# Kernel tuning notes

Hardware: AMD Instinct MI355X
Metric: run time of the kernel (lower is better)

## Reference

```python
import jax, jax.numpy as jnp
import numpy as np

D_MODEL = 1024
N_HEADS = 16
HEAD_DIM = D_MODEL // N_HEADS  # 64
WINDOW = 15
NUM_RANDOM = 2
B, L = 2, 2048


def setup_inputs() -> dict:
    key = jax.random.key(0)
    ks = jax.random.split(key, 5)
    x = jax.random.normal(ks[0], (B, L, D_MODEL), dtype=jnp.float32)
    # rotary angles: theta[t, j] = t / 10000^(2j/head_dim), shape [1, L, head_dim//2]
    inv_freq = 1.0 / (10000.0 ** (jnp.arange(0, HEAD_DIM, 2, dtype=jnp.float32) / HEAD_DIM))
    t = jnp.arange(L, dtype=jnp.float32)
    freqs = (t[:, None] * inv_freq[None, :])[None].astype(jnp.float32)  # [1,L,32]
    scale = 0.02
    wq = jax.random.normal(ks[1], (D_MODEL, D_MODEL), dtype=jnp.float32) * scale
    wk = jax.random.normal(ks[2], (D_MODEL, D_MODEL), dtype=jnp.float32) * scale
    wv = jax.random.normal(ks[3], (D_MODEL, D_MODEL), dtype=jnp.float32) * scale
    wo = jax.random.normal(ks[4], (D_MODEL, D_MODEL), dtype=jnp.float32) * scale
    return {"x": x, "freqs": freqs, "wq": wq, "wk": wk, "wv": wv, "wo": wo}


def _rope(t, cos, sin):
    # t: [B,H,L,hd]; interpret last dim as (hd/2, 2) complex pairs and rotate.
    tr = t.reshape(*t.shape[:-1], -1, 2)
    re, im = tr[..., 0], tr[..., 1]
    out_re = re * cos - im * sin
    out_im = re * sin + im * cos
    return jnp.stack([out_re, out_im], axis=-1).reshape(t.shape)


def _bigbird_mask(Lq):
    ii = jnp.arange(Lq)[:, None]
    jj = jnp.arange(Lq)[None, :]
    causal = jj <= ii
    window = jnp.abs(ii - jj) <= (WINDOW // 2)
    glob = (ii == 0) | (jj == 0)
    # random mask: per row i, NUM_RANDOM indices uniform in [0, i]
    rkey = jax.random.key(42)
    u = jax.random.uniform(rkey, (Lq, NUM_RANDOM))
    ridx = jnp.floor(u * (jnp.arange(Lq, dtype=jnp.float32)[:, None] + 1.0)).astype(jnp.int32)
    rmask = jnp.zeros((Lq, Lq), dtype=bool).at[jnp.arange(Lq)[:, None], ridx].set(True)
    # rows with <= NUM_RANDOM causal options attend to all of them
    rmask = rmask | (causal & (ii < NUM_RANDOM))
    return (causal & (window | rmask)) | glob  # [L,L]


def reference(x, freqs, wq, wk, wv, wo):
    b, l, _ = x.shape
    q = (x @ wq.T).reshape(b, l, N_HEADS, HEAD_DIM).transpose(0, 2, 1, 3)  # [B,H,L,hd]
    k = (x @ wk.T).reshape(b, l, N_HEADS, HEAD_DIM).transpose(0, 2, 1, 3)
    v = (x @ wv.T).reshape(b, l, N_HEADS, HEAD_DIM).transpose(0, 2, 1, 3)
    cos = jnp.cos(freqs[:, :l])[:, None]  # [1,1,L,hd/2]
    sin = jnp.sin(freqs[:, :l])[:, None]
    q = _rope(q, cos, sin)
    k = _rope(k, cos, sin)
    attn_mask = _bigbird_mask(l)  # [L,L], broadcast over B,H
    scale = 1.0 / jnp.sqrt(jnp.float32(HEAD_DIM))
    scores = jnp.einsum("bhqd,bhkd->bhqk", q, k) * scale
    scores = jnp.where(attn_mask[None, None], scores, jnp.finfo(scores.dtype).min)
    p = jax.nn.softmax(scores, axis=-1)
    out = jnp.einsum("bhqk,bhkd->bhqd", p, v)
    out = out.transpose(0, 2, 1, 3).reshape(b, l, D_MODEL)
    return out @ wo.T
```

## Files before the change

kernel.cpp:

```cpp
#include <hip/hip_runtime.h>
#include <math.h>

#define SEQ_L 2048
#define DM 1024
#define NH 16
#define HD 64
#define NB 2
#define KD 1024
#define ND 1024

typedef __bf16 bf16;
typedef __bf16 bf16x8 __attribute__((ext_vector_type(8)));
typedef __bf16 bf16x4 __attribute__((ext_vector_type(4)));
typedef __bf16 bf16x2 __attribute__((ext_vector_type(2)));
typedef float f32x4 __attribute__((ext_vector_type(4)));

__device__ inline uint32_t rotl32(uint32_t v, int n) { return (v << n) | (v >> (32 - n)); }

__device__ inline void threefry(uint32_t x0, uint32_t x1, uint32_t* o0, uint32_t* o1) {
  const uint32_t ks0 = 0u, ks1 = 42u, ks2 = 0u ^ 42u ^ 0x1BD11BDAu;
  x0 += ks0; x1 += ks1;
#define TF_R(rr) { x0 += x1; x1 = rotl32(x1, rr); x1 ^= x0; }
  TF_R(13) TF_R(15) TF_R(26) TF_R(6)
  x0 += ks1; x1 += ks2 + 1u;
  TF_R(17) TF_R(29) TF_R(16) TF_R(24)
  x0 += ks2; x1 += ks0 + 2u;
  TF_R(13) TF_R(15) TF_R(26) TF_R(6)
  x0 += ks0; x1 += ks1 + 3u;
  TF_R(17) TF_R(29) TF_R(16) TF_R(24)
  x0 += ks1; x1 += ks2 + 4u;
  TF_R(13) TF_R(15) TF_R(26) TF_R(6)
  x0 += ks2; x1 += ks0 + 5u;
#undef TF_R
  *o0 = x0; *o1 = x1;
}

__device__ inline int rand_col(int i, int s) {
  uint32_t o0, o1;
  threefry(0u, (uint32_t)(2 * i + s), &o0, &o1);
  uint32_t bits = o0 ^ o1;
  float u = __uint_as_float((bits >> 9) | 0x3f800000u) - 1.0f;
  return (int)floorf(u * (float)(i + 1));
}

__global__ void prep_kernel(const float* __restrict__ x,
                            const float* __restrict__ w0, const float* __restrict__ w1,
                            const float* __restrict__ w2, const float* __restrict__ w3,
                            const float* __restrict__ freqs,
                            bf16* __restrict__ xb,
                            bf16* __restrict__ o0, bf16* __restrict__ o1,
                            bf16* __restrict__ o2, bf16* __restrict__ o3,
                            int* __restrict__ ctab, float2* __restrict__ rtab) {
  const int bx = blockIdx.x;
  const int t = threadIdx.x;
  if (bx < 8192) {
    const float* src;
    bf16* dst;
    int idx;
    if (bx < 4096) { src = x; dst = xb; idx = bx * 256 + t; }
    else {
      int widx = bx - 4096;
      int wsel = widx >> 10;
      switch (wsel) {
        case 0: src = w0; dst = o0; break;
        case 1: src = w1; dst = o1; break;
        case 2: src = w2; dst = o2; break;
        default: src = w3; dst = o3; break;
      }
      idx = (widx & 1023) * 256 + t;
    }
    float4 vv = ((const float4*)src)[idx];
    bf16x4 ov;
    ov[0] = (bf16)vv.x; ov[1] = (bf16)vv.y; ov[2] = (bf16)vv.z; ov[3] = (bf16)vv.w;
    *(bf16x4*)(dst + (size_t)idx * 4) = ov;
    return;
  }
  if (bx < 8200) {
    const int i = (bx - 8192) * 256 + t;
    int cols[11]; int nc = 0;
    if (i >= 1) {
      int lo = i - 7; if (lo < 0) lo = 0;
      for (int j = lo; j <= i; ++j) cols[nc++] = j;
      if (lo > 0) cols[nc++] = 0;
#pragma unroll
      for (int s = 0; s < 2; ++s) {
        int rj = rand_col(i, s);
        bool dup = false;
        for (int c2 = 0; c2 < nc; ++c2) dup |= (cols[c2] == rj);
        if (!dup) cols[nc++] = rj;
      }
    }
    for (int c2 = nc; c2 < 11; ++c2) cols[c2] = -1;
#pragma unroll
    for (int c2 = 0; c2 < 11; ++c2) ctab[i * 12 + c2] = cols[c2];
    ctab[i * 12 + 11] = nc;
    return;
  }
  const int idx = (bx - 8200) * 256 + t;
  float s, c;
  sincosf(freqs[idx], &s, &c);
  rtab[idx] = make_float2(c, s);
}

__device__ inline void gld16(const bf16* g, bf16* l) {
  __builtin_amdgcn_global_load_lds((const __attribute__((address_space(1))) void*)g,
                                   (__attribute__((address_space(3))) void*)l, 16, 0, 0);
}

__device__ inline void gemm_bt_body(const bf16* __restrict__ A, const bf16* __restrict__ W,
                                    bf16* __restrict__ C, const float2* __restrict__ rtab) {
  __shared__ __align__(16) bf16 As[128 * 64];
  __shared__ __align__(16) bf16 Bs[128 * 64];
  const int t = threadIdx.x;
  const int lane = t & 63;
  const int wave = t >> 6;
  const int wm = (wave >> 1) * 64;
  const int wn = (wave & 1) * 64;
  const int m0 = blockIdx.x * 128;
  const int n0 = blockIdx.y * 128;
  const int l15 = lane & 15;
  const int kq = lane >> 4;

  f32x4 acc[4][4] = {};

  for (int k0 = 0; k0 < KD; k0 += 64) {
#pragma unroll
    for (int n = 0; n < 4; ++n) {
      const int s = n * 256 + t;
      const int row = s >> 3;
      const int ch = (s & 7) ^ (row & 7);
      gld16(A + (size_t)(m0 + row) * KD + k0 + ch * 8, As + s * 8);
      gld16(W + (size_t)(n0 + row) * KD + k0 + ch * 8, Bs + s * 8);
    }
    __syncthreads();
#pragma unroll
    for (int ks = 0; ks < 2; ++ks) {
      const int cb = ks * 4 + kq;
      bf16x8 af[4], bfr[4];
#pragma unroll
      for (int mt = 0; mt < 4; ++mt) {
        const int row = wm + mt * 16 + l15;
        af[mt] = *(const bf16x8*)(As + row * 64 + ((cb ^ (row & 7)) * 8));
      }
#pragma unroll
      for (int nt = 0; nt < 4; ++nt) {
        const int row = wn + nt * 16 + l15;
        bfr[nt] = *(const bf16x8*)(Bs + row * 64 + ((cb ^ (row & 7)) * 8));
      }
#pragma unroll
      for (int mt = 0; mt < 4; ++mt)
#pragma unroll
        for (int nt = 0; nt < 4; ++nt)
          acc[mt][nt] = __builtin_amdgcn_mfma_f32_16x16x32_bf16(af[mt], bfr[nt], acc[mt][nt], 0, 0, 0);
    }
    __syncthreads();
  }
  const int colb = n0 + wn + l15;
  const int rowb = m0 + wm + (lane >> 4) * 4;
  const int odd = l15 & 1;
#pragma unroll
  for (int mt = 0; mt < 4; ++mt)
#pragma unroll
    for (int nt = 0; nt < 4; ++nt) {
      const int col = colb + nt * 16;
      const int jj = (col & 63) >> 1;
#pragma unroll
      for (int rr = 0; rr < 4; ++rr) {
        float val = acc[mt][nt][rr];
        float other = __shfl_xor(val, 1);
        if (!odd) {
          const int row = rowb + mt * 16 + rr;
          float lo, hi;
          if (rtab) {
            float2 cs = rtab[(row & (SEQ_L - 1)) * 32 + jj];
            lo = val * cs.x - other * cs.y;
            hi = val * cs.y + other * cs.x;
          } else { lo = val; hi = other; }
          bf16x2 p; p[0] = (bf16)lo; p[1] = (bf16)hi;
          *(bf16x2*)(C + (size_t)row * ND + col) = p;
        }
      }
    }
}

__global__ __launch_bounds__(256, 3) void qkv_gemm_kernel(
    const bf16* __restrict__ xb, const bf16* __restrict__ wqb, const bf16* __restrict__ wkb,
    const bf16* __restrict__ wvb, bf16* __restrict__ qb, bf16* __restrict__ kb, bf16* __restrict__ vb,
    const float2* __restrict__ rtab) {
  const bf16* W = blockIdx.z == 0 ? wqb : blockIdx.z == 1 ? wkb : wvb;
  bf16* O = blockIdx.z == 0 ? qb : blockIdx.z == 1 ? kb : vb;
  const float2* rt = blockIdx.z < 2 ? rtab : nullptr;
  gemm_bt_body(xb, W, O, rt);
}

__global__ __launch_bounds__(256, 2) void out_gemm_kernel(
    bf16* __restrict__ ab, const bf16* __restrict__ wob, float* __restrict__ out,
    const float* __restrict__ pm, const float* __restrict__ pz, const float* __restrict__ pv) {
  const int t = threadIdx.x;
  const int m0 = blockIdx.x * 64;
  const int n0 = blockIdx.y * 128;

  if (blockIdx.x == 0 || blockIdx.x == 32) {
    const int b = blockIdx.x == 0 ? 0 : 1;
#pragma unroll
    for (int e = t; e < DM; e += 256) {
      const int h = e >> 6, d = e & 63;
      const int base = b * 128 + h * 8;
      float M = -1e30f;
#pragma unroll
      for (int c = 0; c < 8; ++c) M = fmaxf(M, pm[base + c]);
      float Z = 0.f, od = 0.f;
#pragma unroll
      for (int c = 0; c < 8; ++c) {
        float sc = __expf(pm[base + c] - M);
        Z += pz[base + c] * sc;
        od += pv[(base + c) * 64 + d] * sc;
      }
      ab[(size_t)b * SEQ_L * DM + e] = (bf16)(od / Z);
    }
    __syncthreads();
  }

  __shared__ __align__(16) bf16 As[64 * 64];
  __shared__ __align__(16) bf16 Bs[128 * 64];
  const int lane = t & 63;
  const int wave = t >> 6;
  const int wm = (wave >> 1) * 32;
  const int wn = (wave & 1) * 64;
  const int l15 = lane & 15;
  const int kq = lane >> 4;

  f32x4 acc[2][4] = {};

  for (int k0 = 0; k0 < KD; k0 += 64) {
#pragma unroll
    for (int n = 0; n < 2; ++n) {
      const int s = n * 256 + t;
      const int row = s >> 3;
      const int ch = (s & 7) ^ (row & 7);
      gld16(ab + (size_t)(m0 + row) * KD + k0 + ch * 8, As + s * 8);
    }
#pragma unroll
    for (int n = 0; n < 4; ++n) {
      const int s = n * 256 + t;
      const int row = s >> 3;
      const int ch = (s & 7) ^ (row & 7);
      gld16(wob + (size_t)(n0 + row) * KD + k0 + ch * 8, Bs + s * 8);
    }
    __syncthreads();
#pragma unroll
    for (int ks = 0; ks < 2; ++ks) {
      const int cb = ks * 4 + kq;
      bf16x8 af[2], bfr[4];
#pragma unroll
      for (int mt = 0; mt < 2; ++mt) {
        const int row = wm + mt * 16 + l15;
        af[mt] = *(const bf16x8*)(As + row * 64 + ((cb ^ (row & 7)) * 8));
      }
#pragma unroll
      for (int nt = 0; nt < 4; ++nt) {
        const int row = wn + nt * 16 + l15;
        bfr[nt] = *(const bf16x8*)(Bs + row * 64 + ((cb ^ (row & 7)) * 8));
      }
#pragma unroll
      for (int mt = 0; mt < 2; ++mt)
#pragma unroll
        for (int nt = 0; nt < 4; ++nt)
          acc[mt][nt] = __builtin_amdgcn_mfma_f32_16x16x32_bf16(af[mt], bfr[nt], acc[mt][nt], 0, 0, 0);
    }
    __syncthreads();
  }
  const int colb = n0 + wn + l15;
  const int rowb = m0 + wm + (lane >> 4) * 4;
#pragma unroll
  for (int mt = 0; mt < 2; ++mt)
#pragma unroll
    for (int nt = 0; nt < 4; ++nt)
#pragma unroll
      for (int rr = 0; rr < 4; ++rr)
        out[(size_t)(rowb + mt * 16 + rr) * ND + colb + nt * 16] = acc[mt][nt][rr];
}

__global__ __launch_bounds__(256, 2) void attn_kernel(const bf16* __restrict__ q, const bf16* __restrict__ k,
                                                      const bf16* __restrict__ v, bf16* __restrict__ o,
                                                      const int* __restrict__ ctab,
                                                      float* __restrict__ pm, float* __restrict__ pz,
                                                      float* __restrict__ pv) {
  const int t = threadIdx.x;
  const int lane = t & 63;
  const int w = t >> 6;

  __shared__ float sbuf[256];
  __shared__ float redm[4], redz[4];
  __shared__ float part[4][64];

  if (blockIdx.x >= 256) {
    const int sbx = blockIdx.x - 256;
    const int b = sbx >> 9;
    const int tt = sbx & 511;
    const int tile = ((tt & 7) << 6) + (tt >> 3);
    const int i = tile * 4 + 1 + w;
    if (i >= SEQ_L) return;
    const size_t bb = (size_t)b * SEQ_L * DM;
    const int eo = lane * 16;

    const bf16* qrow = q + bb + (size_t)i * DM + eo;
    bf16x8 qv0 = *(const bf16x8*)(qrow);
    bf16x8 qv1 = *(const bf16x8*)(qrow + 8);

    const int4* cp = (const int4*)(ctab + i * 12);
    int4 ca = cp[0], cb = cp[1], cc = cp[2];
    int cols[11] = {ca.x, ca.y, ca.z, ca.w, cb.x, cb.y, cb.z, cb.w, cc.x, cc.y, cc.z};

    bf16x8 kv[11][2], vv[11][2];
#pragma unroll
    for (int c = 0; c < 11; ++c) {
      int cj = cols[c] < 0 ? 0 : cols[c];
      const bf16* krow = k + bb + (size_t)cj * DM + eo;
      kv[c][0] = *(const bf16x8*)(krow);
      kv[c][1] = *(const bf16x8*)(krow + 8);
    }
#pragma unroll
    for (int c = 0; c < 11; ++c) {
      int cj = cols[c] < 0 ? 0 : cols[c];
      const bf16* vrow = v + bb + (size_t)cj * DM + eo;
      vv[c][0] = *(const bf16x8*)(vrow);
      vv[c][1] = *(const bf16x8*)(vrow + 8);
    }

    float sv[11];
#pragma unroll
    for (int c = 0; c < 11; ++c) {
      float acc = 0.f;
#pragma unroll
      for (int e = 0; e < 8; ++e)
        acc += (float)qv0[e] * (float)kv[c][0][e] + (float)qv1[e] * (float)kv[c][1][e];
      sv[c] = acc;
    }
#pragma unroll
    for (int c = 0; c < 11; ++c) {
      sv[c] += __shfl_xor(sv[c], 1);
      sv[c] += __shfl_xor(sv[c], 2);
      sv[c] = cols[c] < 0 ? -1e30f : sv[c] * 0.125f;
    }
    float m = -1e30f;
#pragma unroll
    for (int c = 0; c < 11; ++c) m = fmaxf(m, sv[c]);
    float z = 0.f;
#pragma unroll
    for (int c = 0; c < 11; ++c) { sv[c] = __expf(sv[c] - m); z += sv[c]; }
    const float inv = 1.f / z;

    float oa[16] = {};
#pragma unroll
    for (int c = 0; c < 11; ++c) {
#pragma unroll
      for (int e = 0; e < 8; ++e) {
        oa[e]     += sv[c] * (float)vv[c][0][e];
        oa[8 + e] += sv[c] * (float)vv[c][1][e];
      }
    }
    bf16x8 ov0, ov1;
#pragma unroll
    for (int e = 0; e < 8; ++e) {
      ov0[e] = (bf16)(oa[e] * inv);
      ov1[e] = (bf16)(oa[8 + e] * inv);
    }
    bf16* orow = o + bb + (size_t)i * DM + eo;
    *(bf16x8*)(orow) = ov0;
    *(bf16x8*)(orow + 8) = ov1;
    return;
  }

  const int idx = blockIdx.x;
  const int b = idx >> 7;
  const int rem = idx & 127;
  const int h = rem >> 3;
  const int c = rem & 7;
  const size_t hb = (size_t)b * SEQ_L * DM + (size_t)h * HD;
  const int j = c * 256 + t;

  bf16x8 qv8[8];
#pragma unroll
  for (int cc = 0; cc < 8; ++cc) qv8[cc] = *(const bf16x8*)(q + hb + cc * 8);

  float acc = 0.f;
#pragma unroll
  for (int cc = 0; cc < 8; ++cc) {
    bf16x8 kv = *(const bf16x8*)(k + hb + (size_t)j * DM + cc * 8);
#pragma unroll
    for (int e = 0; e < 8; ++e) acc += (float)qv8[cc][e] * (float)kv[e];
  }
  float s = acc * 0.125f;
  float mloc = s;
#pragma unroll
  for (int off = 32; off > 0; off >>= 1) mloc = fmaxf(mloc, __shfl_xor(mloc, off));
  if (lane == 0) redm[w] = mloc;
  __syncthreads();
  const float m = fmaxf(fmaxf(redm[0], redm[1]), fmaxf(redm[2], redm[3]));

  float e = __expf(s - m);
  sbuf[t] = e;
  float zloc = e;
#pragma unroll
  for (int off = 32; off > 0; off >>= 1) zloc += __shfl_xor(zloc, off);
  if (lane == 0) redz[w] = zloc;
  __syncthreads();
  const float zc = redz[0] + redz[1] + redz[2] + redz[3];

  float oa = 0.f;
  for (int jj = w; jj < 256; jj += 4)
    oa += sbuf[jj] * (float)v[hb + (size_t)(c * 256 + jj) * DM + lane];
  part[w][lane] = oa;
  __syncthreads();
  if (t < 64) pv[idx * 64 + t] = part[0][t] + part[1][t] + part[2][t] + part[3][t];
  if (t == 0) { pm[idx] = m; pz[idx] = zc; }
}

extern "C" void kernel_launch(void* const* d_in, const int* in_sizes, int n_in,
                              void* d_out, int out_size, void* d_ws, size_t ws_size,
                              hipStream_t stream) {
  const float* x     = (const float*)d_in[0];
  const float* freqs = (const float*)d_in[1];
  const float* wq    = (const float*)d_in[2];
  const float* wk    = (const float*)d_in[3];
  const float* wv    = (const float*)d_in[4];
  const float* wo    = (const float*)d_in[5];
  float* out = (float*)d_out;

  char* ws = (char*)d_ws;
  bf16* xb  = (bf16*)(ws + 0);
  bf16* wqb = (bf16*)(ws + 8388608);
  bf16* wkb = (bf16*)(ws + 10485760);
  bf16* wvb = (bf16*)(ws + 12582912);
  bf16* wob = (bf16*)(ws + 14680064);
  bf16* qb  = (bf16*)(ws + 16777216);
  bf16* kb  = (bf16*)(ws + 25165824);
  bf16* vb  = (bf16*)(ws + 33554432);
  bf16* ab  = (bf16*)(ws + 41943040);
  int*    ctab = (int*)(ws + 50331648);
  float*  pm   = (float*)(ws + 50462720);
  float*  pz   = (float*)(ws + 50463744);
  float*  pv   = (float*)(ws + 50464768);
  float2* rtab = (float2*)(ws + 50593792);
  (void)ws_size;

  prep_kernel<<<8456, 256, 0, stream>>>(x, wq, wk, wv, wo, freqs, xb, wqb, wkb, wvb, wob, ctab, rtab);
  qkv_gemm_kernel<<<dim3(32, 8, 3), 256, 0, stream>>>(xb, wqb, wkb, wvb, qb, kb, vb, rtab);
  attn_kernel<<<dim3(1280, 1), 256, 0, stream>>>(qb, kb, vb, ab, ctab, pm, pz, pv);
  out_gemm_kernel<<<dim3(64, 8), 256, 0, stream>>>(ab, wob, out, pm, pz, pv);
}
```

Before: 164.6 us.

## Fuse Q/K/V projections into one GEMM block sharing the x tile

The QKV projection kernel now has each block load one 128x64 tile of x and multiply it against 64-column tiles of all three weight matrices, instead of launching separate blocks per weight. This cuts redundant x loads from global memory into LDS and turns a 768-block 3D grid into a 512-block 2D grid. In exchange each block holds more accumulators (24 MFMA tiles), and launch bounds drop from 3 to 2 blocks per SM, which may lower occupancy.

```diff
diff --git a/kernel.cpp b/kernel.cpp
--- a/kernel.cpp
+++ b/kernel.cpp
@@ -107,21 +107,26 @@
                                    (__attribute__((address_space(3))) void*)l, 16, 0, 0);
 }
 
-__device__ inline void gemm_bt_body(const bf16* __restrict__ A, const bf16* __restrict__ W,
-                                    bf16* __restrict__ C, const float2* __restrict__ rtab) {
+__global__ __launch_bounds__(256, 2) void qkv_gemm_kernel(
+    const bf16* __restrict__ xb, const bf16* __restrict__ wqb, const bf16* __restrict__ wkb,
+    const bf16* __restrict__ wvb, bf16* __restrict__ qb, bf16* __restrict__ kb, bf16* __restrict__ vb,
+    const float2* __restrict__ rtab) {
   __shared__ __align__(16) bf16 As[128 * 64];
-  __shared__ __align__(16) bf16 Bs[128 * 64];
+  __shared__ __align__(16) bf16 Bs[3][64 * 64];
+  const bf16* Ws[3] = {wqb, wkb, wvb};
+  bf16* Ds[3] = {qb, kb, vb};
+
   const int t = threadIdx.x;
   const int lane = t & 63;
-  const int wave = t >> 6;
-  const int wm = (wave >> 1) * 64;
-  const int wn = (wave & 1) * 64;
+  const int w = t >> 6;
+  const int wm = (w >> 1) * 64;
+  const int wn = (w & 1) * 32;
   const int m0 = blockIdx.x * 128;
-  const int n0 = blockIdx.y * 128;
+  const int n0 = blockIdx.y * 64;
   const int l15 = lane & 15;
   const int kq = lane >> 4;
 
-  f32x4 acc[4][4] = {};
+  f32x4 acc[3][4][2] = {};
 
   for (int k0 = 0; k0 < KD; k0 += 64) {
 #pragma unroll
@@ -129,29 +134,41 @@
       const int s = n * 256 + t;
       const int row = s >> 3;
       const int ch = (s & 7) ^ (row & 7);
-      gld16(A + (size_t)(m0 + row) * KD + k0 + ch * 8, As + s * 8);
-      gld16(W + (size_t)(n0 + row) * KD + k0 + ch * 8, Bs + s * 8);
-    }
+      gld16(xb + (size_t)(m0 + row) * KD + k0 + ch * 8, As + s * 8);
+    }
+#pragma unroll
+    for (int j = 0; j < 3; ++j)
+#pragma unroll
+      for (int n = 0; n < 2; ++n) {
+        const int s = n * 256 + t;
+        const int row = s >> 3;
+        const int ch = (s & 7) ^ (row & 7);
+        gld16(Ws[j] + (size_t)(n0 + row) * KD + k0 + ch * 8, &Bs[j][s * 8]);
+      }
     __syncthreads();
 #pragma unroll
     for (int ks = 0; ks < 2; ++ks) {
       const int cb = ks * 4 + kq;
-      bf16x8 af[4], bfr[4];
+      bf16x8 af[4];
 #pragma unroll
       for (int mt = 0; mt < 4; ++mt) {
         const int row = wm + mt * 16 + l15;
         af[mt] = *(const bf16x8*)(As + row * 64 + ((cb ^ (row & 7)) * 8));
       }
 #pragma unroll
-      for (int nt = 0; nt < 4; ++nt) {
-        const int row = wn + nt * 16 + l15;
-        bfr[nt] = *(const bf16x8*)(Bs + row * 64 + ((cb ^ (row & 7)) * 8));
-      }
-#pragma unroll
-      for (int mt = 0; mt < 4; ++mt)
-#pragma unroll
-        for (int nt = 0; nt < 4; ++nt)
-          acc[mt][nt] = __builtin_amdgcn_mfma_f32_16x16x32_bf16(af[mt], bfr[nt], acc[mt][nt], 0, 0, 0);
+      for (int j = 0; j < 3; ++j) {
+        bf16x8 bfr[2];
+#pragma unroll
+        for (int nt = 0; nt < 2; ++nt) {
+          const int row = wn + nt * 16 + l15;
+          bfr[nt] = *(const bf16x8*)(&Bs[j][row * 64 + ((cb ^ (row & 7)) * 8)]);
+        }
+#pragma unroll
+        for (int mt = 0; mt < 4; ++mt)
+#pragma unroll
+          for (int nt = 0; nt < 2; ++nt)
+            acc[j][mt][nt] = __builtin_amdgcn_mfma_f32_16x16x32_bf16(af[mt], bfr[nt], acc[j][mt][nt], 0, 0, 0);
+      }
     }
     __syncthreads();
   }
@@ -159,38 +176,33 @@
   const int rowb = m0 + wm + (lane >> 4) * 4;
   const int odd = l15 & 1;
 #pragma unroll
-  for (int mt = 0; mt < 4; ++mt)
-#pragma unroll
-    for (int nt = 0; nt < 4; ++nt) {
-      const int col = colb + nt * 16;
-      const int jj = (col & 63) >> 1;
-#pragma unroll
-      for (int rr = 0; rr < 4; ++rr) {
-        float val = acc[mt][nt][rr];
-        float other = __shfl_xor(val, 1);
-        if (!odd) {
-          const int row = rowb + mt * 16 + rr;
-          float lo, hi;
-          if (rtab) {
-            float2 cs = rtab[(row & (SEQ_L - 1)) * 32 + jj];
-            lo = val * cs.x - other * cs.y;
-            hi = val * cs.y + other * cs.x;
-          } else { lo = val; hi = other; }
-          bf16x2 p; p[0] = (bf16)lo; p[1] = (bf16)hi;
-          *(bf16x2*)(C + (size_t)row * ND + col) = p;
+  for (int j = 0; j < 3; ++j) {
+    bf16* D = Ds[j];
+    const bool dorope = (j < 2);
+#pragma unroll
+    for (int mt = 0; mt < 4; ++mt)
+#pragma unroll
+      for (int nt = 0; nt < 2; ++nt) {
+        const int col = colb + nt * 16;
+        const int jj = (col & 63) >> 1;
+#pragma unroll
+        for (int rr = 0; rr < 4; ++rr) {
+          float val = acc[j][mt][nt][rr];
+          float other = __shfl_xor(val, 1);
+          if (!odd) {
+            const int row = rowb + mt * 16 + rr;
+            float lo, hi;
+            if (dorope) {
+              float2 cs = rtab[(row & (SEQ_L - 1)) * 32 + jj];
+              lo = val * cs.x - other * cs.y;
+              hi = val * cs.y + other * cs.x;
+            } else { lo = val; hi = other; }
+            bf16x2 p; p[0] = (bf16)lo; p[1] = (bf16)hi;
+            *(bf16x2*)(D + (size_t)row * ND + col) = p;
+          }
         }
       }
-    }
-}
-
-__global__ __launch_bounds__(256, 3) void qkv_gemm_kernel(
-    const bf16* __restrict__ xb, const bf16* __restrict__ wqb, const bf16* __restrict__ wkb,
-    const bf16* __restrict__ wvb, bf16* __restrict__ qb, bf16* __restrict__ kb, bf16* __restrict__ vb,
-    const float2* __restrict__ rtab) {
-  const bf16* W = blockIdx.z == 0 ? wqb : blockIdx.z == 1 ? wkb : wvb;
-  bf16* O = blockIdx.z == 0 ? qb : blockIdx.z == 1 ? kb : vb;
-  const float2* rt = blockIdx.z < 2 ? rtab : nullptr;
-  gemm_bt_body(xb, W, O, rt);
+  }
 }
 
 __global__ __launch_bounds__(256, 2) void out_gemm_kernel(
@@ -446,7 +458,7 @@
   (void)ws_size;
 
   prep_kernel<<<8456, 256, 0, stream>>>(x, wq, wk, wv, wo, freqs, xb, wqb, wkb, wvb, wob, ctab, rtab);
-  qkv_gemm_kernel<<<dim3(32, 8, 3), 256, 0, stream>>>(xb, wqb, wkb, wvb, qb, kb, vb, rtab);
+  qkv_gemm_kernel<<<dim3(32, 16), 256, 0, stream>>>(xb, wqb, wkb, wvb, qb, kb, vb, rtab);
   attn_kernel<<<dim3(1280, 1), 256, 0, stream>>>(qb, kb, vb, ab, ctab, pm, pz, pv);
   out_gemm_kernel<<<dim3(64, 8), 256, 0, stream>>>(ab, wob, out, pm, pz, pv);
 }
```

Result: faster. 161.3 us (-2.0%).
